# Optimization experiments

Hardware: AMD Instinct MI355X
Metric: run time of the kernel (lower is better)

Reference implementation:

```python
import jax, jax.numpy as jnp
import numpy as np

# Model dims (match init_kwargs)
H = 16        # num query heads
HKV = 4       # num key/value heads
D = 128       # head dim
HID = H * D   # hidden size = 2048
W = 4         # ring world size; we simulate rank W-1 (sees all kv shards)
SL = 2048     # local (per-rank) sequence length


def _block_attn(q, kb, vb, scale, causal):
    # q: [B,H,Sl,D], kb/vb: [B,H,Sl,D]
    S = jnp.einsum('bhqd,bhkd->bhqk', q, kb) * scale
    if causal:
        mask = jnp.triu(jnp.ones((q.shape[2], kb.shape[2]), dtype=bool), k=1)
        S = jnp.where(mask[None, None], -jnp.inf, S)
    S_max = jnp.max(S, axis=-1, keepdims=True)
    exp_S = jnp.exp(S - S_max)
    exp_sum = jnp.sum(exp_S, axis=-1, keepdims=True)
    lse = jnp.log(exp_sum) + S_max            # [B,H,Sl,1]
    O = jnp.einsum('bhqk,bhkd->bhqd', exp_S / exp_sum, vb)
    return O, lse


def _ring_attention_fwd(x_q, x_kv, Wq, Wk, Wv, Wo):
    B, Sl, hid = x_q.shape
    n_rep = H // HKV
    scale = 1.0 / np.sqrt(D).astype(np.float32)

    q = (x_q @ Wq.T).reshape(B, Sl, H, D).transpose(0, 2, 1, 3)          # [B,H,Sl,D]
    k = (x_kv @ Wk.T).reshape(B, -1, HKV, D).transpose(0, 2, 1, 3)       # [B,Hkv,Stot,D]
    v = (x_kv @ Wv.T).reshape(B, -1, HKV, D).transpose(0, 2, 1, 3)
    # repeat_kv (GQA)
    k = jnp.repeat(k, n_rep, axis=1)                                     # [B,H,Stot,D]
    v = jnp.repeat(v, n_rep, axis=1)
    # split kv into W ring shards along sequence
    kb = k.reshape(B, H, W, Sl, D)
    vb = v.reshape(B, H, W, Sl, D)

    out, lse = None, None
    rank = W - 1
    for step in range(W):  # fixed small ring loop
        blk = rank - step  # shard held at this ring step (own shard first)
        bo, blse = _block_attn(q, kb[:, :, blk], vb[:, :, blk], scale, causal=(step == 0))
        if out is None:
            out, lse = bo, blse
        else:
            # online merge (matches update_out_and_lse)
            out = out - jax.nn.sigmoid(blse - lse) * (out - bo)
            lse = lse - jax.nn.log_sigmoid(lse - blse)

    out = out.transpose(0, 2, 1, 3).reshape(B, Sl, H * D)
    return out @ Wo.T


def setup_inputs() -> dict:
    key = jax.random.key(0)
    ks = jax.random.split(key, 6)
    s = 0.02
    return {
        'x_q': jax.random.normal(ks[0], (1, SL, HID), dtype=jnp.float32),
        'x_kv': jax.random.normal(ks[1], (1, W * SL, HID), dtype=jnp.float32),
        'Wq': jax.random.normal(ks[2], (HID, HID), dtype=jnp.float32) * s,
        'Wk': jax.random.normal(ks[3], (HKV * D, HID), dtype=jnp.float32) * s,
        'Wv': jax.random.normal(ks[4], (HKV * D, HID), dtype=jnp.float32) * s,
        'Wo': jax.random.normal(ks[5], (HID, HID), dtype=jnp.float32) * s,
    }


def reference(x_q, x_kv, Wq, Wk, Wv, Wo):
    return _ring_attention_fwd(x_q, x_kv, Wq, Wk, Wv, Wo)
```

## Files before the change

### kernel.cpp

```cpp
#include <hip/hip_runtime.h>
#include <stdint.h>

typedef unsigned short u16;
typedef short bf16x8 __attribute__((ext_vector_type(8)));
typedef float f32x4 __attribute__((ext_vector_type(4)));
typedef float f32x16 __attribute__((ext_vector_type(16)));

#define MFMA16(a, b, c) __builtin_amdgcn_mfma_f32_16x16x32_bf16(a, b, c, 0, 0, 0)
#define MFMA32(a, b, c) __builtin_amdgcn_mfma_f32_32x32x16_bf16(a, b, c, 0, 0, 0)

__device__ __forceinline__ void ld_lds16(const void* g, void* l) {
  __builtin_amdgcn_global_load_lds(
      (const __attribute__((address_space(1))) void*)(uint64_t)(uintptr_t)g,
      (__attribute__((address_space(3))) void*)(uint32_t)(uintptr_t)l,
      16, 0, 0);
}

__device__ __forceinline__ u16 f32_to_bf16(float f) {
  uint32_t u = __float_as_uint(f);
  return (u16)((u + 0x7FFFu + ((u >> 16) & 1u)) >> 16);
}

__device__ __forceinline__ uint32_t cvt_pk_bf16(float a, float b) {
  uint32_t r;
  asm("v_cvt_pk_bf16_f32 %0, %1, %2" : "=v"(r) : "v"(a), "v"(b));
  return r;
}

__device__ __forceinline__ void perm_swap(uint32_t& x, uint32_t& y) {
  asm volatile("v_permlane32_swap_b32 %0, %1" : "+v"(x), "+v"(y));
}

__global__ void cvt_all(const float* __restrict__ xq, const float* __restrict__ xkv,
                        const float* __restrict__ Wq, const float* __restrict__ Wk,
                        const float* __restrict__ Wv, const float* __restrict__ Wo,
                        u16* __restrict__ xq_b, u16* __restrict__ xkv_b,
                        u16* __restrict__ wq_b, u16* __restrict__ wk_b,
                        u16* __restrict__ wv_b, u16* __restrict__ wo_b) {
  const int M4 = 1 << 20;
  const int total = 7 * M4 + (M4 >> 1);
  int i = blockIdx.x * blockDim.x + threadIdx.x;
  int stride = gridDim.x * blockDim.x;
  for (; i < total; i += stride) {
    const float* src;
    u16* dst;
    int off;
    if (i < M4)                         { src = xq;  dst = xq_b;  off = i; }
    else if (i < 5 * M4)                { src = xkv; dst = xkv_b; off = i - M4; }
    else if (i < 6 * M4)                { src = Wq;  dst = wq_b;  off = i - 5 * M4; }
    else if (i < 6 * M4 + (M4 >> 2))    { src = Wk;  dst = wk_b;  off = i - 6 * M4; }
    else if (i < 6 * M4 + (M4 >> 1))    { src = Wv;  dst = wv_b;  off = i - 6 * M4 - (M4 >> 2); }
    else                                { src = Wo;  dst = wo_b;  off = i - 6 * M4 - (M4 >> 1); }
    float4 v = reinterpret_cast<const float4*>(src)[off];
    ushort4 o;
    o.x = f32_to_bf16(v.x); o.y = f32_to_bf16(v.y);
    o.z = f32_to_bf16(v.z); o.w = f32_to_bf16(v.w);
    reinterpret_cast<ushort4*>(dst)[off] = o;
  }
}

__device__ __forceinline__ void gemm_body(const u16* __restrict__ A,
                                          const u16* __restrict__ B,
                                          void* __restrict__ Cv, int M, int N,
                                          int K, float alpha, int bx, int by,
                                          int outf32, u16* lA, u16* lB) {
  const int tid = threadIdx.x;
  const int lane = tid & 63;
  const int w = tid >> 6;
  const int c = lane & 15, g = lane >> 4;
  const int wm = (w & 1) * 64, wn = (w >> 1) * 32;
  const int m0 = by * 128, n0 = bx * 64;
  const int sr = tid >> 3, sc = tid & 7;

  f32x4 acc[4][2] = {};

  for (int k0 = 0; k0 < K; k0 += 64) {
    __syncthreads();
#pragma unroll
    for (int p = 0; p < 4; ++p) {
      int row = p * 32 + sr;
      int gc = sc ^ (row & 7);
      ld_lds16(A + (size_t)(m0 + row) * K + k0 + gc * 8, &lA[row * 64 + sc * 8]);
    }
#pragma unroll
    for (int p = 0; p < 2; ++p) {
      int idx = p * 256 + tid;
      int row = idx >> 3, cc = idx & 7;
      int gc = cc ^ (row & 7);
      ld_lds16(B + (size_t)(n0 + row) * K + k0 + gc * 8, &lB[row * 64 + cc * 8]);
    }
    __syncthreads();
#pragma unroll
    for (int kc = 0; kc < 2; ++kc) {
      bf16x8 a[4], b[2];
#pragma unroll
      for (int t = 0; t < 4; ++t) {
        int row = wm + t * 16 + c;
        int ch = (g + 4 * kc) ^ (row & 7);
        a[t] = *(const bf16x8*)&lA[row * 64 + ch * 8];
      }
#pragma unroll
      for (int t = 0; t < 2; ++t) {
        int row = wn + t * 16 + c;
        int ch = (g + 4 * kc) ^ (row & 7);
        b[t] = *(const bf16x8*)&lB[row * 64 + ch * 8];
      }
#pragma unroll
      for (int i = 0; i < 4; ++i)
#pragma unroll
        for (int j = 0; j < 2; ++j)
          acc[i][j] = MFMA16(a[i], b[j], acc[i][j]);
    }
  }

#pragma unroll
  for (int i = 0; i < 4; ++i)
#pragma unroll
    for (int j = 0; j < 2; ++j)
#pragma unroll
      for (int r = 0; r < 4; ++r) {
        int mm = m0 + wm + i * 16 + g * 4 + r;
        int nn = n0 + wn + j * 16 + c;
        float v = acc[i][j][r] * alpha;
        if (outf32)
          ((float*)Cv)[(size_t)mm * N + nn] = v;
        else
          ((u16*)Cv)[(size_t)mm * N + nn] = f32_to_bf16(v);
      }
}

__global__ __launch_bounds__(256, 4)
void gemm3(const u16* __restrict__ xq_b, const u16* __restrict__ wq_b,
           u16* __restrict__ Qb, const u16* __restrict__ xkv_b,
           const u16* __restrict__ wk_b, u16* __restrict__ Kb,
           const u16* __restrict__ wv_b, u16* __restrict__ VTb, float qscale) {
  __shared__ u16 lA[128 * 64];
  __shared__ u16 lB[64 * 64];
  int b = blockIdx.x;
  if (b < 512) {
    gemm_body(xq_b, wq_b, Qb, 2048, 2048, 2048, qscale, b & 31, b >> 5, 0, lA, lB);
  } else if (b < 1024) {
    b -= 512;
    gemm_body(xkv_b, wk_b, Kb, 8192, 512, 2048, 1.0f, b & 7, b >> 3, 0, lA, lB);
  } else {
    b -= 1024;
    gemm_body(wv_b, xkv_b, VTb, 512, 8192, 2048, 1.0f, b & 127, b >> 7, 0, lA, lB);
  }
}

__global__ __launch_bounds__(256, 4)
void gemm_out(const u16* __restrict__ A, const u16* __restrict__ B,
              float* __restrict__ Cv) {
  __shared__ u16 lA[128 * 64];
  __shared__ u16 lB[64 * 64];
  gemm_body(A, B, Cv, 2048, 2048, 2048, 1.0f, blockIdx.x, blockIdx.y, 1, lA, lB);
}

__global__ __launch_bounds__(256, 2)
void attn_kernel(const u16* __restrict__ Q, const u16* __restrict__ Kg,
                 const u16* __restrict__ VT, float* __restrict__ Opart,
                 float* __restrict__ mlp) {
  __shared__ u16 lK[2][64 * 128];
  __shared__ u16 lV[2][128 * 64];

  const int tid = threadIdx.x;
  const int w = tid >> 6, lane = tid & 63;
  const int ql = lane & 31, hi = lane >> 5;
  const int bx = blockIdx.x;
  const int h = bx & 15, kvs = bx >> 8;
  const int qbr = (bx >> 4) & 15;
  const int qb = kvs ? qbr : 15 - qbr;
  const int hk = h >> 2;
  const int i0 = qb * 128;
  const int q0 = i0 + w * 32;

  const int nt = ((i0 + 6271) >> 6) + 1;
  const int nth = nt >> 1;
  const int t0 = kvs ? nth : 0;
  const int ntt = (kvs ? nt : nth) - t0;

  bf16x8 qf[8];
#pragma unroll
  for (int kc = 0; kc < 8; ++kc)
    qf[kc] = *(const bf16x8*)&Q[(size_t)(q0 + ql) * 2048 + h * 128 + kc * 16 + hi * 8];

  bf16x8 onesB;
#pragma unroll
  for (int i = 0; i < 8; ++i) onesB[i] = (short)0x3F80;

  f32x16 a[4] = {};
  f32x16 lacc = {};

  auto stage = [&](int buf, int t) {
    const int j0 = t << 6;
#pragma unroll
    for (int p = 0; p < 4; ++p) {
      int idx = p * 256 + tid;
      int row = idx >> 4, cc = idx & 15;
      int gc = cc ^ (row & 15);
      ld_lds16(Kg + (size_t)(j0 + row) * 512 + hk * 128 + gc * 8,
               &lK[buf][row * 128 + cc * 8]);
    }
#pragma unroll
    for (int p = 0; p < 4; ++p) {
      int idx = p * 256 + tid;
      int row = idx >> 3, cc = idx & 7;
      int gc = cc ^ (row & 7);
      ld_lds16(VT + (size_t)(hk * 128 + row) * 8192 + j0 + gc * 8,
               &lV[buf][row * 64 + cc * 8]);
    }
  };

  stage(0, t0);

  for (int it = 0; it < ntt; ++it) {
    const int curb = it & 1;
    const int j0 = (t0 + it) << 6;
    if (it + 1 < ntt) {
      stage(curb ^ 1, t0 + it + 1);
      asm volatile("s_waitcnt vmcnt(8)" ::: "memory");
    } else {
      asm volatile("s_waitcnt vmcnt(0)" ::: "memory");
    }
    __builtin_amdgcn_s_barrier();

    f32x16 s0 = {}, s1 = {};
    __builtin_amdgcn_s_setprio(1);
#pragma unroll
    for (int kc = 0; kc < 8; ++kc) {
      int ch = kc * 2 + hi;
      bf16x8 kfa = *(const bf16x8*)&lK[curb][ql * 128 + (ch ^ (ql & 15)) * 8];
      bf16x8 kfb = *(const bf16x8*)&lK[curb][(32 + ql) * 128 + (ch ^ (ql & 15)) * 8];
      s0 = MFMA32(kfa, qf[kc], s0);
      s1 = MFMA32(kfb, qf[kc], s1);
    }
    __builtin_amdgcn_s_setprio(0);

    if (j0 + 63 > q0 + 6144) {
#pragma unroll
      for (int r = 0; r < 16; ++r) {
        int jrow = (r & 3) + 8 * (r >> 2) + 4 * hi;
        if (j0 + jrow > q0 + ql + 6144) s0[r] = -1e30f;
        if (j0 + 32 + jrow > q0 + ql + 6144) s1[r] = -1e30f;
      }
    }

#pragma unroll
    for (int r = 0; r < 16; ++r) {
      s0[r] = __builtin_amdgcn_exp2f(s0[r]);
      s1[r] = __builtin_amdgcn_exp2f(s1[r]);
    }

    bf16x8 pbf[4];
#pragma unroll
    for (int jt = 0; jt < 2; ++jt) {
      const f32x16& sv = jt ? s1 : s0;
      uint32_t A0 = cvt_pk_bf16(sv[0], sv[1]);
      uint32_t B0 = cvt_pk_bf16(sv[4], sv[5]);
      perm_swap(A0, B0);
      uint32_t A1 = cvt_pk_bf16(sv[2], sv[3]);
      uint32_t B1 = cvt_pk_bf16(sv[6], sv[7]);
      perm_swap(A1, B1);
      uint32_t A2 = cvt_pk_bf16(sv[8], sv[9]);
      uint32_t B2 = cvt_pk_bf16(sv[12], sv[13]);
      perm_swap(A2, B2);
      uint32_t A3 = cvt_pk_bf16(sv[10], sv[11]);
      uint32_t B3 = cvt_pk_bf16(sv[14], sv[15]);
      perm_swap(A3, B3);
      union { uint32_t u[4]; bf16x8 v; } pa, pb;
      pa.u[0] = A0; pa.u[1] = A1; pa.u[2] = B0; pa.u[3] = B1;
      pb.u[0] = A2; pb.u[1] = A3; pb.u[2] = B2; pb.u[3] = B3;
      pbf[2 * jt] = pa.v;
      pbf[2 * jt + 1] = pb.v;
    }

    __builtin_amdgcn_s_setprio(1);
    lacc = MFMA32(pbf[0], onesB, lacc);
    lacc = MFMA32(pbf[1], onesB, lacc);
    lacc = MFMA32(pbf[2], onesB, lacc);
    lacc = MFMA32(pbf[3], onesB, lacc);
#pragma unroll
    for (int kc = 0; kc < 4; ++kc)
#pragma unroll
      for (int dt = 0; dt < 4; ++dt) {
        int row = dt * 32 + ql;
        int ch = (kc * 2 + hi) ^ (row & 7);
        bf16x8 vf = *(const bf16x8*)&lV[curb][row * 64 + ch * 8];
        a[dt] = MFMA32(pbf[kc], vf, a[dt]);
      }
    __builtin_amdgcn_s_setprio(0);

    __builtin_amdgcn_s_barrier();
  }

  const size_t pbase = ((size_t)(kvs * 16 + h) * 16 + qb);
  float* Op = Opart + pbase * 16384;
  float* mlb = mlp + pbase * 256;
#pragma unroll
  for (int dt = 0; dt < 4; ++dt)
#pragma unroll
    for (int r = 0; r < 16; ++r) {
      int qrow = w * 32 + (r & 3) + 8 * (r >> 2) + 4 * hi;
      Op[(size_t)qrow * 128 + dt * 32 + ql] = a[dt][r];
    }
  if (ql == 0) {
#pragma unroll
    for (int r = 0; r < 16; ++r)
      mlb[128 + w * 32 + (r & 3) + 8 * (r >> 2) + 4 * hi] = lacc[r];
  }
}

__global__ __launch_bounds__(256)
void attn_merge(const float* __restrict__ Opart, const float* __restrict__ mlp,
                u16* __restrict__ O) {
  const int bx = blockIdx.x;
  const int h = bx >> 4, qb = bx & 15;
  const int q = threadIdx.x & 127, hf = threadIdx.x >> 7;
  const size_t p0 = ((size_t)(0 + h) * 16 + qb);
  const size_t p1 = ((size_t)(16 + h) * 16 + qb);
  float ll0 = mlp[p0 * 256 + 128 + q], ll1 = mlp[p1 * 256 + 128 + q];
  float inv = 1.f / (ll0 + ll1);
  const float* A = Opart + p0 * 16384 + (size_t)q * 128 + hf * 64;
  const float* B = Opart + p1 * 16384 + (size_t)q * 128 + hf * 64;
  u16* out = O + (size_t)(qb * 128 + q) * 2048 + h * 128 + hf * 64;
#pragma unroll
  for (int d = 0; d < 64; d += 4) {
    float4 a = *(const float4*)&A[d];
    float4 b = *(const float4*)&B[d];
    ushort4 o;
    o.x = f32_to_bf16((a.x + b.x) * inv);
    o.y = f32_to_bf16((a.y + b.y) * inv);
    o.z = f32_to_bf16((a.z + b.z) * inv);
    o.w = f32_to_bf16((a.w + b.w) * inv);
    *(ushort4*)&out[d] = o;
  }
}

extern "C" void kernel_launch(void* const* d_in, const int* in_sizes, int n_in,
                              void* d_out, int out_size, void* d_ws, size_t ws_size,
                              hipStream_t stream) {
  (void)in_sizes; (void)n_in; (void)out_size; (void)ws_size;
  const float* xq = (const float*)d_in[0];
  const float* xkv = (const float*)d_in[1];
  const float* Wq = (const float*)d_in[2];
  const float* Wk = (const float*)d_in[3];
  const float* Wv = (const float*)d_in[4];
  const float* Wo = (const float*)d_in[5];

  u16* ws = (u16*)d_ws;
  const size_t M1 = 1024 * 1024;
  u16* xq_b  = ws;
  u16* xkv_b = ws + 4 * M1;
  u16* wq_b  = ws + 20 * M1;
  u16* wk_b  = ws + 24 * M1;
  u16* wv_b  = ws + 25 * M1;
  u16* wo_b  = ws + 26 * M1;
  u16* Qb    = ws + 30 * M1;
  u16* Kb    = ws + 34 * M1;
  u16* VTb   = ws + 38 * M1;
  u16* Ob    = ws + 42 * M1;
  float* Opart = (float*)d_ws;
  float* mlptr = Opart + 8388608;

  cvt_all<<<2048, 256, 0, stream>>>(xq, xkv, Wq, Wk, Wv, Wo,
                                    xq_b, xkv_b, wq_b, wk_b, wv_b, wo_b);

  gemm3<<<1536, 256, 0, stream>>>(xq_b, wq_b, Qb, xkv_b, wk_b, Kb, wv_b, VTb,
                                  0.12752837f);

  attn_kernel<<<512, 256, 0, stream>>>(Qb, Kb, VTb, Opart, mlptr);
  attn_merge<<<256, 256, 0, stream>>>(Opart, mlptr, Ob);

  gemm_out<<<dim3(32, 16), 256, 0, stream>>>(Ob, wo_b, (float*)d_out);
}
```

Before: 277.9 us.

## Split attention tile loop into unmasked main and masked tail, interleave halves

New measurement: 275.2 us (median of 3 runs). About the same (-1.0%).

```diff
diff --git a/kernel.cpp b/kernel.cpp
--- a/kernel.cpp
+++ b/kernel.cpp
@@ -178,6 +178,10 @@
   const int nth = nt >> 1;
   const int t0 = kvs ? nth : 0;
   const int ntt = (kvs ? nt : nth) - t0;
+  const int tsafe = (i0 + 6081) >> 6;
+  int nmain = tsafe + 1 - t0;
+  if (nmain > ntt) nmain = ntt;
+  if (nmain < 0) nmain = 0;
 
   bf16x8 qf[8];
 #pragma unroll
@@ -211,87 +215,106 @@
     }
   };
 
+  auto finish = [&](f32x16& sv, bf16x8& pA, bf16x8& pB) {
+#pragma unroll
+    for (int r = 0; r < 16; ++r) sv[r] = __builtin_amdgcn_exp2f(sv[r]);
+    uint32_t A0 = cvt_pk_bf16(sv[0], sv[1]);
+    uint32_t B0 = cvt_pk_bf16(sv[4], sv[5]);
+    perm_swap(A0, B0);
+    uint32_t A1 = cvt_pk_bf16(sv[2], sv[3]);
+    uint32_t B1 = cvt_pk_bf16(sv[6], sv[7]);
+    perm_swap(A1, B1);
+    uint32_t A2 = cvt_pk_bf16(sv[8], sv[9]);
+    uint32_t B2 = cvt_pk_bf16(sv[12], sv[13]);
+    perm_swap(A2, B2);
+    uint32_t A3 = cvt_pk_bf16(sv[10], sv[11]);
+    uint32_t B3 = cvt_pk_bf16(sv[14], sv[15]);
+    perm_swap(A3, B3);
+    union { uint32_t u[4]; bf16x8 v; } pa, pb;
+    pa.u[0] = A0; pa.u[1] = A1; pa.u[2] = B0; pa.u[3] = B1;
+    pb.u[0] = A2; pb.u[1] = A3; pb.u[2] = B2; pb.u[3] = B3;
+    pA = pa.v;
+    pB = pb.v;
+  };
+
   stage(0, t0);
 
-  for (int it = 0; it < ntt; ++it) {
-    const int curb = it & 1;
-    const int j0 = (t0 + it) << 6;
-    if (it + 1 < ntt) {
-      stage(curb ^ 1, t0 + it + 1);
-      asm volatile("s_waitcnt vmcnt(8)" ::: "memory");
-    } else {
-      asm volatile("s_waitcnt vmcnt(0)" ::: "memory");
-    }
-    __builtin_amdgcn_s_barrier();
-
-    f32x16 s0 = {}, s1 = {};
-    __builtin_amdgcn_s_setprio(1);
-#pragma unroll
-    for (int kc = 0; kc < 8; ++kc) {
-      int ch = kc * 2 + hi;
-      bf16x8 kfa = *(const bf16x8*)&lK[curb][ql * 128 + (ch ^ (ql & 15)) * 8];
-      bf16x8 kfb = *(const bf16x8*)&lK[curb][(32 + ql) * 128 + (ch ^ (ql & 15)) * 8];
-      s0 = MFMA32(kfa, qf[kc], s0);
-      s1 = MFMA32(kfb, qf[kc], s1);
-    }
-    __builtin_amdgcn_s_setprio(0);
-
-    if (j0 + 63 > q0 + 6144) {
-#pragma unroll
-      for (int r = 0; r < 16; ++r) {
-        int jrow = (r & 3) + 8 * (r >> 2) + 4 * hi;
-        if (j0 + jrow > q0 + ql + 6144) s0[r] = -1e30f;
-        if (j0 + 32 + jrow > q0 + ql + 6144) s1[r] = -1e30f;
-      }
-    }
-
-#pragma unroll
-    for (int r = 0; r < 16; ++r) {
-      s0[r] = __builtin_amdgcn_exp2f(s0[r]);
-      s1[r] = __builtin_amdgcn_exp2f(s1[r]);
-    }
-
-    bf16x8 pbf[4];
-#pragma unroll
-    for (int jt = 0; jt < 2; ++jt) {
-      const f32x16& sv = jt ? s1 : s0;
-      uint32_t A0 = cvt_pk_bf16(sv[0], sv[1]);
-      uint32_t B0 = cvt_pk_bf16(sv[4], sv[5]);
-      perm_swap(A0, B0);
-      uint32_t A1 = cvt_pk_bf16(sv[2], sv[3]);
-      uint32_t B1 = cvt_pk_bf16(sv[6], sv[7]);
-      perm_swap(A1, B1);
-      uint32_t A2 = cvt_pk_bf16(sv[8], sv[9]);
-      uint32_t B2 = cvt_pk_bf16(sv[12], sv[13]);
-      perm_swap(A2, B2);
-      uint32_t A3 = cvt_pk_bf16(sv[10], sv[11]);
-      uint32_t B3 = cvt_pk_bf16(sv[14], sv[15]);
-      perm_swap(A3, B3);
-      union { uint32_t u[4]; bf16x8 v; } pa, pb;
-      pa.u[0] = A0; pa.u[1] = A1; pa.u[2] = B0; pa.u[3] = B1;
-      pb.u[0] = A2; pb.u[1] = A3; pb.u[2] = B2; pb.u[3] = B3;
-      pbf[2 * jt] = pa.v;
-      pbf[2 * jt + 1] = pb.v;
-    }
-
-    __builtin_amdgcn_s_setprio(1);
-    lacc = MFMA32(pbf[0], onesB, lacc);
-    lacc = MFMA32(pbf[1], onesB, lacc);
-    lacc = MFMA32(pbf[2], onesB, lacc);
-    lacc = MFMA32(pbf[3], onesB, lacc);
-#pragma unroll
-    for (int kc = 0; kc < 4; ++kc)
-#pragma unroll
-      for (int dt = 0; dt < 4; ++dt) {
-        int row = dt * 32 + ql;
-        int ch = (kc * 2 + hi) ^ (row & 7);
-        bf16x8 vf = *(const bf16x8*)&lV[curb][row * 64 + ch * 8];
-        a[dt] = MFMA32(pbf[kc], vf, a[dt]);
-      }
-    __builtin_amdgcn_s_setprio(0);
-
-    __builtin_amdgcn_s_barrier();
-  }
+  int it = 0;
+  auto run_tiles = [&](int end, bool domask) {
+    for (; it < end; ++it) {
+      const int curb = it & 1;
+      const int j0 = (t0 + it) << 6;
+      if (it + 1 < ntt) {
+        stage(curb ^ 1, t0 + it + 1);
+        asm volatile("s_waitcnt vmcnt(8)" ::: "memory");
+      } else {
+        asm volatile("s_waitcnt vmcnt(0)" ::: "memory");
+      }
+      __builtin_amdgcn_s_barrier();
+
+      f32x16 s0 = {}, s1 = {};
+      bf16x8 pbf[4];
+      __builtin_amdgcn_s_setprio(1);
+#pragma unroll
+      for (int kc = 0; kc < 8; ++kc) {
+        int ch = kc * 2 + hi;
+        bf16x8 kfa = *(const bf16x8*)&lK[curb][ql * 128 + (ch ^ (ql & 15)) * 8];
+        s0 = MFMA32(kfa, qf[kc], s0);
+      }
+      __builtin_amdgcn_s_setprio(0);
+#pragma unroll
+      for (int kc = 0; kc < 8; ++kc) {
+        int ch = kc * 2 + hi;
+        bf16x8 kfb = *(const bf16x8*)&lK[curb][(32 + ql) * 128 + (ch ^ (ql & 15)) * 8];
+        s1 = MFMA32(kfb, qf[kc], s1);
+      }
+      if (domask) {
+#pragma unroll
+        for (int r = 0; r < 16; ++r) {
+          int jrow = (r & 3) + 8 * (r >> 2) + 4 * hi;
+          if (j0 + jrow > q0 + ql + 6144) s0[r] = -1e30f;
+        }
+      }
+      finish(s0, pbf[0], pbf[1]);
+      lacc = MFMA32(pbf[0], onesB, lacc);
+      lacc = MFMA32(pbf[1], onesB, lacc);
+#pragma unroll
+      for (int kc = 0; kc < 2; ++kc)
+#pragma unroll
+        for (int dt = 0; dt < 4; ++dt) {
+          int row = dt * 32 + ql;
+          int ch = (kc * 2 + hi) ^ (row & 7);
+          bf16x8 vf = *(const bf16x8*)&lV[curb][row * 64 + ch * 8];
+          a[dt] = MFMA32(pbf[kc], vf, a[dt]);
+        }
+      if (domask) {
+#pragma unroll
+        for (int r = 0; r < 16; ++r) {
+          int jrow = (r & 3) + 8 * (r >> 2) + 4 * hi;
+          if (j0 + 32 + jrow > q0 + ql + 6144) s1[r] = -1e30f;
+        }
+      }
+      finish(s1, pbf[2], pbf[3]);
+      __builtin_amdgcn_s_setprio(1);
+      lacc = MFMA32(pbf[2], onesB, lacc);
+      lacc = MFMA32(pbf[3], onesB, lacc);
+#pragma unroll
+      for (int kc = 2; kc < 4; ++kc)
+#pragma unroll
+        for (int dt = 0; dt < 4; ++dt) {
+          int row = dt * 32 + ql;
+          int ch = (kc * 2 + hi) ^ (row & 7);
+          bf16x8 vf = *(const bf16x8*)&lV[curb][row * 64 + ch * 8];
+          a[dt] = MFMA32(pbf[kc], vf, a[dt]);
+        }
+      __builtin_amdgcn_s_setprio(0);
+
+      __builtin_amdgcn_s_barrier();
+    }
+  };
+
+  run_tiles(nmain, false);
+  run_tiles(ntt, true);
 
   const size_t pbase = ((size_t)(kvs * 16 + h) * 16 + qb);
   float* Op = Opart + pbase * 16384;
```
